# Kernel tuning notes

Hardware: AMD Instinct MI355X
Metric: run time of the kernel (lower is better)

The kernel has to match this reference:

```python
import jax, jax.numpy as jnp
import numpy as np

N, H, E, T, ED, AB = 50000, 64, 800000, 800000, 64, 16


def setup_inputs() -> dict:
    key = jax.random.key(0)
    ks = jax.random.split(key, 26)

    def nrm(k, shape, scale=1.0):
        return jax.random.normal(k, shape, dtype=jnp.float32) * scale

    d = {}
    d["s"] = nrm(ks[0], (N, H))
    d["v"] = nrm(ks[1], (N, H, 3))
    d["edge_index"] = jax.random.randint(ks[2], (2, E), 0, N, dtype=jnp.int32)
    d["edge_rbf"] = jax.random.uniform(ks[3], (E, ED), dtype=jnp.float32)
    raw_dir = jax.random.normal(ks[4], (E, 3), dtype=jnp.float32)
    d["edge_dir"] = raw_dir / jnp.linalg.norm(raw_dir, axis=-1, keepdims=True)
    d["triplet_kj"] = jax.random.randint(ks[5], (T,), 0, E, dtype=jnp.int32)
    d["triplet_ji"] = jax.random.randint(ks[6], (T,), 0, E, dtype=jnp.int32)
    d["angle_feat"] = jax.random.uniform(ks[7], (T, AB), dtype=jnp.float32)

    def lin(kw, kb, fan_in, fan_out):
        sc = 1.0 / np.sqrt(fan_in)
        return nrm(kw, (fan_in, fan_out), sc), nrm(kb, (fan_out,), sc)

    d["W_t1"], d["b_t1"] = lin(ks[8], ks[9], 2 * ED + AB, H)
    d["W_t2"], d["b_t2"] = lin(ks[10], ks[11], H, H)
    d["W_m1"], d["b_m1"] = lin(ks[12], ks[13], 2 * H + ED + H, H)
    d["W_m2"], d["b_m2"] = lin(ks[14], ks[15], H, 2 * H)
    d["W_u1"], d["b_u1"] = lin(ks[16], ks[17], 3 * H, H)
    d["W_u2"], d["b_u2"] = lin(ks[18], ks[19], H, H)
    d["W_g1"], d["b_g1"] = lin(ks[20], ks[21], 3 * H, H)
    d["W_g2"], d["b_g2"] = lin(ks[22], ks[23], H, H)
    d["ln_g"] = jnp.ones((H,), jnp.float32)
    d["ln_b"] = jnp.zeros((H,), jnp.float32)
    return d


def _mlp(x, W1, b1, W2, b2):
    return jax.nn.silu(x @ W1 + b1) @ W2 + b2


def reference(s, v, edge_index, edge_rbf, edge_dir, triplet_kj, triplet_ji,
              angle_feat, W_t1, b_t1, W_t2, b_t2, W_m1, b_m1, W_m2, b_m2,
              W_u1, b_u1, W_u2, b_u2, W_g1, b_g1, W_g2, b_g2, ln_g, ln_b):
    n_nodes, hid = s.shape
    n_edges = edge_rbf.shape[0]

    # 3-body triplet messages: gather two edge rbf rows + angle feature
    t_in = jnp.concatenate([edge_rbf[triplet_kj], edge_rbf[triplet_ji], angle_feat], axis=-1)
    t_msg = _mlp(t_in, W_t1, b_t1, W_t2, b_t2)                 # [T, H]
    angle_agg = jax.ops.segment_sum(t_msg, triplet_ji, num_segments=n_edges)  # [E, H]

    src, dst = edge_index[0], edge_index[1]
    msg_in = jnp.concatenate([s[src], s[dst], edge_rbf, angle_agg], axis=-1)  # [E, 4H]
    msg = _mlp(msg_in, W_m1, b_m1, W_m2, b_m2)                 # [E, 2H]
    m_s, m_v_coeff = jnp.split(msg, 2, axis=-1)

    agg_s = jax.ops.segment_sum(m_s, dst, num_segments=n_nodes)  # [N, H]
    m_v = m_v_coeff[:, :, None] * edge_dir[:, None, :]          # [E, H, 3]
    agg_v = jax.ops.segment_sum(m_v.reshape(n_edges, hid * 3), dst,
                                num_segments=n_nodes).reshape(n_nodes, hid, 3)

    v_norm = jnp.linalg.norm(v, axis=-1)                        # [N, H]
    ctx = jnp.concatenate([s, agg_s, v_norm], axis=-1)          # [N, 3H]
    s_new = s + _mlp(ctx, W_u1, b_u1, W_u2, b_u2)
    gate = jax.nn.sigmoid(_mlp(ctx, W_g1, b_g1, W_g2, b_g2))
    v_new = v + gate[..., None] * agg_v

    mu = s_new.mean(axis=-1, keepdims=True)
    var = s_new.var(axis=-1, keepdims=True)
    s_ln = (s_new - mu) / jnp.sqrt(var + 1e-5) * ln_g + ln_b
    s_out = jax.nn.silu(s_ln)
    return (s_out, v_new)
```

## Files before the change

kernel.cpp:

```cpp
#include <hip/hip_runtime.h>
#include <cstdint>
#include <cstddef>

#define NN 50000
#define NE 800000
#define NT 800000

typedef unsigned short u16;
typedef unsigned int u32;
typedef __attribute__((ext_vector_type(8))) short short8;
typedef __attribute__((ext_vector_type(4))) float f32x4;

__device__ __forceinline__ float silu_f(float x) { return x / (1.f + __expf(-x)); }
__device__ __forceinline__ float sigm_f(float x) { return 1.f / (1.f + __expf(-x)); }
__device__ __forceinline__ u16 f2b(float x) {
  u32 u = __float_as_uint(x);
  u32 r = u + 0x7fffu + ((u >> 16) & 1u);
  return (u16)(r >> 16);
}
__device__ __forceinline__ float b2f(u16 h) { return __uint_as_float(((u32)h) << 16); }
__device__ __forceinline__ u32 pk2(float a, float b) {
  return (u32)f2b(a) | ((u32)f2b(b) << 16);
}

template <int RW>
__device__ __forceinline__ int lx(int r, int c) {
  return r * RW + ((((c >> 3) ^ (r & 7)) << 3) | (c & 7));
}

__global__ __launch_bounds__(256) void kcvt_hist(
    const float* __restrict__ erbf, u16* __restrict__ erbf_bf,
    const float* __restrict__ s, u16* __restrict__ s_bf,
    const int* __restrict__ tji, const int* __restrict__ edst,
    int* __restrict__ tcnt, int* __restrict__ ncnt) {
  int i = blockIdx.x * 256 + threadIdx.x;
  const int NCVT = (NE + NN) * 16;
  if (i < NCVT) {
    const float* in; u16* out; int j;
    if (i < NE * 16) { in = erbf; out = erbf_bf; j = i; }
    else { in = s; out = s_bf; j = i - NE * 16; }
    float4 v = ((const float4*)in)[j];
    uint2 p;
    p.x = pk2(v.x, v.y);
    p.y = pk2(v.z, v.w);
    ((uint2*)out)[j] = p;
  } else {
    int j = i - NCVT;
    if (j < NT) atomicAdd(&tcnt[tji[j]], 1);
    else {
      j -= NT;
      if (j < NE) atomicAdd(&ncnt[edst[j]], 1);
    }
  }
}

__global__ __launch_bounds__(256) void kscan1b(
    const int* __restrict__ inA, int nA, int* __restrict__ outA, int* __restrict__ bsA, int BA,
    const int* __restrict__ inB, int nB, int* __restrict__ outB, int* __restrict__ bsB) {
  __shared__ int sh[256];
  const int* in; int n; int* out; int* bs; int blk;
  if ((int)blockIdx.x < BA) { in = inA; n = nA; out = outA; bs = bsA; blk = blockIdx.x; }
  else { in = inB; n = nB; out = outB; bs = bsB; blk = blockIdx.x - BA; }
  int tid = threadIdx.x;
  size_t base = (size_t)blk * 1024;
  int v[4];
  int acc = 0;
#pragma unroll
  for (int q = 0; q < 4; ++q) {
    size_t i = base + (size_t)tid * 4 + q;
    int x = (i < (size_t)n) ? in[i] : 0;
    v[q] = acc;
    acc += x;
  }
  sh[tid] = acc;
  __syncthreads();
  for (int off = 1; off < 256; off <<= 1) {
    int y = (tid >= off) ? sh[tid - off] : 0;
    __syncthreads();
    sh[tid] += y;
    __syncthreads();
  }
  int excl = (tid == 0) ? 0 : sh[tid - 1];
  if (tid == 255) bs[blk] = sh[255];
#pragma unroll
  for (int q = 0; q < 4; ++q) {
    size_t i = base + (size_t)tid * 4 + q;
    if (i < (size_t)n) out[i] = excl + v[q];
  }
}

__global__ __launch_bounds__(1024) void kscan2b(int* __restrict__ bsA, int nbA,
                                                int* __restrict__ bsB, int nbB) {
  __shared__ int sh[1024];
  int* bs = (blockIdx.x == 0) ? bsA : bsB;
  int nb = (blockIdx.x == 0) ? nbA : nbB;
  int tid = threadIdx.x;
  sh[tid] = (tid < nb) ? bs[tid] : 0;
  __syncthreads();
  for (int off = 1; off < 1024; off <<= 1) {
    int y = (tid >= off) ? sh[tid - off] : 0;
    __syncthreads();
    sh[tid] += y;
    __syncthreads();
  }
  if (tid < nb) bs[tid] = (tid == 0) ? 0 : sh[tid - 1];
}

__global__ __launch_bounds__(256) void kscan3b(
    int* __restrict__ outA, const int* __restrict__ bsA, int nA, int totalA,
    int* __restrict__ outB, const int* __restrict__ bsB, int nB, int totalB) {
  int i = blockIdx.x * 256 + threadIdx.x;
  if (i <= nA) {
    if (i < nA) outA[i] += bsA[i >> 10];
    else outA[nA] = totalA;
  } else {
    int j = i - (nA + 1);
    if (j < nB) outB[j] += bsB[j >> 10];
    else if (j == nB) outB[nB] = totalB;
  }
}

__global__ __launch_bounds__(256) void kprep_all(
    const int* __restrict__ tji, const int* __restrict__ toff, int* __restrict__ tcnt,
    int* __restrict__ tids, const float* __restrict__ afeat, u16* __restrict__ afeat_s,
    const int* __restrict__ edst, const int* __restrict__ noff, int* __restrict__ ncnt,
    int* __restrict__ eslot, const float* __restrict__ dir, float* __restrict__ dir_s,
    const float* __restrict__ Wt1, const float* __restrict__ Wt2,
    const float* __restrict__ Wm1, const float* __restrict__ Wm2,
    const float* __restrict__ Wu1, const float* __restrict__ Wu2,
    const float* __restrict__ Wg1, const float* __restrict__ Wg2,
    u16* __restrict__ Pt1, u16* __restrict__ Pt2,
    u16* __restrict__ Pm1, u16* __restrict__ Pm2,
    u16* __restrict__ Pu1, u16* __restrict__ Pu2,
    u16* __restrict__ Pg1, u16* __restrict__ Pg2) {
  int i = blockIdx.x * 256 + threadIdx.x;
  if (i < NT) {
    int k = tji[i];
    int slot = toff[k] + (atomicSub(&tcnt[k], 1) - 1);
    tids[slot] = i;
    const float4* src = (const float4*)(afeat + (size_t)i * 16);
    uint2* dst = (uint2*)(afeat_s + (size_t)slot * 16);
#pragma unroll
    for (int q = 0; q < 4; ++q) {
      float4 v = src[q];
      uint2 p;
      p.x = pk2(v.x, v.y);
      p.y = pk2(v.z, v.w);
      dst[q] = p;
    }
  } else if (i < NT + NE) {
    int j = i - NT;
    int k = edst[j];
    int slot = noff[k] + (atomicSub(&ncnt[k], 1) - 1);
    eslot[j] = slot;
    dir_s[(size_t)slot * 3 + 0] = dir[(size_t)j * 3 + 0];
    dir_s[(size_t)slot * 3 + 1] = dir[(size_t)j * 3 + 1];
    dir_s[(size_t)slot * 3 + 2] = dir[(size_t)j * 3 + 2];
  } else {
    int g = i - NT - NE;
    int f = g >> 6, l = g & 63;
    const float* W; u16* out; int K, N, fl;
    if (f < 20)       { W = Wt1; out = Pt1; K = 144; N = 64;  fl = f; }
    else if (f < 28)  { W = Wt2; out = Pt2; K = 64;  N = 64;  fl = f - 20; }
    else if (f < 60)  { W = Wm1; out = Pm1; K = 256; N = 64;  fl = f - 28; }
    else if (f < 76)  { W = Wm2; out = Pm2; K = 64;  N = 128; fl = f - 60; }
    else if (f < 100) { W = Wu1; out = Pu1; K = 192; N = 64;  fl = f - 76; }
    else if (f < 108) { W = Wu2; out = Pu2; K = 64;  N = 64;  fl = f - 100; }
    else if (f < 132) { W = Wg1; out = Pg1; K = 192; N = 64;  fl = f - 108; }
    else if (f < 140) { W = Wg2; out = Pg2; K = 64;  N = 64;  fl = f - 132; }
    else return;
    int nt = fl % (N / 16);
    int kt = fl / (N / 16);
    int k0 = kt * 32 + (l >> 4) * 8;
    int n = nt * 16 + (l & 15);
    u16 vals[8];
#pragma unroll
    for (int j = 0; j < 8; ++j) {
      int kk = k0 + j;
      vals[j] = (kk < K) ? f2b(W[(size_t)kk * N + n]) : (u16)0;
    }
    uint4* dst = (uint4*)(out + (size_t)fl * 512 + l * 8);
    uint4 p;
    p.x = (u32)vals[0] | ((u32)vals[1] << 16);
    p.y = (u32)vals[2] | ((u32)vals[3] << 16);
    p.z = (u32)vals[4] | ((u32)vals[5] << 16);
    p.w = (u32)vals[6] | ((u32)vals[7] << 16);
    *dst = p;
  }
}

__global__ __launch_bounds__(256) void ktrip_mfma(
    const int* __restrict__ tkj, const int* __restrict__ tji,
    const u16* __restrict__ erbf_bf, const u16* __restrict__ afeat_s,
    const int* __restrict__ tids,
    const u16* __restrict__ Wp1, const float* __restrict__ b1,
    const u16* __restrict__ Wp2, const float* __restrict__ b2,
    u16* __restrict__ tmsg_s) {
  __shared__ __align__(16) u16 Xs[64 * 192];
  u16* Hs = Xs + 64 * 128;
  const int tid = threadIdx.x;
  const int l = tid & 63;
  const int w = tid >> 6;
  const int st0 = blockIdx.x * 64;

#pragma unroll
  for (int it = 0; it < 4; ++it) {
    int idx = it * 256 + tid;
    int sel = idx >> 9, r = (idx >> 3) & 63, ch = idx & 7;
    int t = tids[st0 + r];
    int node = sel ? tji[t] : tkj[t];
    uint4 vv = *(const uint4*)&erbf_bf[(size_t)node * 64 + ch * 8];
    *(uint4*)&Xs[lx<192>(r, sel * 64 + ch * 8)] = vv;
  }
  {
    int r = tid >> 2, c = (tid & 3) * 4;
    uint2 p2 = *(const uint2*)&afeat_s[(size_t)(st0 + r) * 16 + c];
    *(uint2*)&Xs[lx<192>(r, 128 + c)] = p2;
  }
#pragma unroll
  for (int i = 0; i < 2; ++i) {
    int idx = i * 256 + tid;
    int r = idx >> 3, c = 144 + (idx & 7) * 2;
    *(u32*)&Xs[lx<192>(r, c)] = 0;
  }
  __syncthreads();

  f32x4 acc1[4];
  {
    float bias = b1[w * 16 + (l & 15)];
#pragma unroll
    for (int mt = 0; mt < 4; ++mt) acc1[mt] = (f32x4){bias, bias, bias, bias};
    for (int ks = 0; ks < 5; ++ks) {
      short8 bf = *(const short8*)(Wp1 + ((size_t)(ks * 4 + w) * 64 + l) * 8);
#pragma unroll
      for (int mt = 0; mt < 4; ++mt) {
        short8 af = *(const short8*)&Xs[lx<192>(mt * 16 + (l & 15), ks * 32 + ((l >> 4) << 3))];
        acc1[mt] = __builtin_amdgcn_mfma_f32_16x16x32_bf16(af, bf, acc1[mt], 0, 0, 0);
      }
    }
  }
  __syncthreads();
#pragma unroll
  for (int mt = 0; mt < 4; ++mt)
#pragma unroll
    for (int q = 0; q < 4; ++q) {
      int r = mt * 16 + (l >> 4) * 4 + q;
      Hs[lx<64>(r, w * 16 + (l & 15))] = f2b(silu_f(acc1[mt][q]));
    }
  __syncthreads();

  f32x4 acc2[4];
  {
    float bias = b2[w * 16 + (l & 15)];
#pragma unroll
    for (int mt = 0; mt < 4; ++mt) acc2[mt] = (f32x4){bias, bias, bias, bias};
    for (int ks = 0; ks < 2; ++ks) {
      short8 bf = *(const short8*)(Wp2 + ((size_t)(ks * 4 + w) * 64 + l) * 8);
#pragma unroll
      for (int mt = 0; mt < 4; ++mt) {
        short8 af = *(const short8*)&Hs[lx<64>(mt * 16 + (l & 15), ks * 32 + ((l >> 4) << 3))];
        acc2[mt] = __builtin_amdgcn_mfma_f32_16x16x32_bf16(af, bf, acc2[mt], 0, 0, 0);
      }
    }
  }
  __syncthreads();
#pragma unroll
  for (int mt = 0; mt < 4; ++mt)
#pragma unroll
    for (int q = 0; q < 4; ++q) {
      int r = mt * 16 + (l >> 4) * 4 + q;
      Xs[lx<64>(r, w * 16 + (l & 15))] = f2b(acc2[mt][q]);
    }
  __syncthreads();
  for (int i = 0; i < 2; ++i) {
    int idx = i * 256 + tid;
    int r = idx >> 3, c0 = (idx & 7) << 3;
    uint4 val = *(const uint4*)&Xs[lx<64>(r, c0)];
    *(uint4*)(tmsg_s + (size_t)(st0 + r) * 64 + c0) = val;
  }
}

__global__ __launch_bounds__(256) void kmsg_mfma(
    const int* __restrict__ eidx, const u16* __restrict__ s_bf,
    const u16* __restrict__ erbf_bf,
    const int* __restrict__ toff, const u16* __restrict__ tmsg_s,
    const int* __restrict__ eslot,
    const u16* __restrict__ Wp1, const float* __restrict__ b1,
    const u16* __restrict__ Wp2, const float* __restrict__ b2,
    u16* __restrict__ msg_s) {
  __shared__ __align__(16) u16 Xs[64 * 256];
  u16* Hs = Xs + 64 * 192;
  const int tid = threadIdx.x;
  const int l = tid & 63;
  const int w = tid >> 6;
  const int e0 = blockIdx.x * 64;

#pragma unroll
  for (int i = 0; i < 2; ++i) {
    int idx = i * 256 + tid;
    int r = idx >> 3, c0 = (idx & 7) << 3;
    uint4 vv = *(const uint4*)&erbf_bf[(size_t)(e0 + r) * 64 + c0];
    *(uint4*)&Xs[lx<256>(r, 128 + c0)] = vv;
  }
#pragma unroll
  for (int it = 0; it < 4; ++it) {
    int idx = it * 256 + tid;
    int sel = idx >> 9, r = (idx >> 3) & 63, ch = idx & 7;
    int node = eidx[sel * NE + e0 + r];
    uint4 vv = *(const uint4*)&s_bf[(size_t)node * 64 + ch * 8];
    *(uint4*)&Xs[lx<256>(r, sel * 64 + ch * 8)] = vv;
  }
#pragma unroll
  for (int it = 0; it < 2; ++it) {
    int idx = it * 256 + tid;
    int r = idx >> 3, ch = idx & 7;
    int e = e0 + r;
    int r0 = toff[e], r1 = toff[e + 1];
    float a[8];
#pragma unroll
    for (int j = 0; j < 8; ++j) a[j] = 0.f;
    for (int ri = r0; ri < r1; ++ri) {
      uint4 pk = *(const uint4*)&tmsg_s[(size_t)ri * 64 + ch * 8];
      a[0] += b2f((u16)(pk.x & 0xffff)); a[1] += b2f((u16)(pk.x >> 16));
      a[2] += b2f((u16)(pk.y & 0xffff)); a[3] += b2f((u16)(pk.y >> 16));
      a[4] += b2f((u16)(pk.z & 0xffff)); a[5] += b2f((u16)(pk.z >> 16));
      a[6] += b2f((u16)(pk.w & 0xffff)); a[7] += b2f((u16)(pk.w >> 16));
    }
    uint4 p;
    p.x = pk2(a[0], a[1]);
    p.y = pk2(a[2], a[3]);
    p.z = pk2(a[4], a[5]);
    p.w = pk2(a[6], a[7]);
    *(uint4*)&Xs[lx<256>(r, 192 + ch * 8)] = p;
  }
  __syncthreads();

  f32x4 acc1[4];
  {
    float bias = b1[w * 16 + (l & 15)];
#pragma unroll
    for (int mt = 0; mt < 4; ++mt) acc1[mt] = (f32x4){bias, bias, bias, bias};
    for (int ks = 0; ks < 8; ++ks) {
      short8 bf = *(const short8*)(Wp1 + ((size_t)(ks * 4 + w) * 64 + l) * 8);
#pragma unroll
      for (int mt = 0; mt < 4; ++mt) {
        short8 af = *(const short8*)&Xs[lx<256>(mt * 16 + (l & 15), ks * 32 + ((l >> 4) << 3))];
        acc1[mt] = __builtin_amdgcn_mfma_f32_16x16x32_bf16(af, bf, acc1[mt], 0, 0, 0);
      }
    }
  }
  __syncthreads();
#pragma unroll
  for (int mt = 0; mt < 4; ++mt)
#pragma unroll
    for (int q = 0; q < 4; ++q) {
      int r = mt * 16 + (l >> 4) * 4 + q;
      Hs[lx<64>(r, w * 16 + (l & 15))] = f2b(silu_f(acc1[mt][q]));
    }
  __syncthreads();

  f32x4 acc2[2][4];
#pragma unroll
  for (int pp = 0; pp < 2; ++pp) {
    int nt = w * 2 + pp;
    float bias = b2[nt * 16 + (l & 15)];
#pragma unroll
    for (int mt = 0; mt < 4; ++mt) acc2[pp][mt] = (f32x4){bias, bias, bias, bias};
    for (int ks = 0; ks < 2; ++ks) {
      short8 bf = *(const short8*)(Wp2 + ((size_t)(ks * 8 + nt) * 64 + l) * 8);
#pragma unroll
      for (int mt = 0; mt < 4; ++mt) {
        short8 af = *(const short8*)&Hs[lx<64>(mt * 16 + (l & 15), ks * 32 + ((l >> 4) << 3))];
        acc2[pp][mt] = __builtin_amdgcn_mfma_f32_16x16x32_bf16(af, bf, acc2[pp][mt], 0, 0, 0);
      }
    }
  }
  __syncthreads();
#pragma unroll
  for (int pp = 0; pp < 2; ++pp)
#pragma unroll
    for (int mt = 0; mt < 4; ++mt)
#pragma unroll
      for (int q = 0; q < 4; ++q) {
        int r = mt * 16 + (l >> 4) * 4 + q;
        Xs[lx<128>(r, (w * 2 + pp) * 16 + (l & 15))] = f2b(acc2[pp][mt][q]);
      }
  __syncthreads();
  for (int i = 0; i < 4; ++i) {
    int idx = i * 256 + tid;
    int r = idx >> 4, c0 = (idx & 15) << 3;
    int slot = eslot[e0 + r];
    uint4 val = *(const uint4*)&Xs[lx<128>(r, c0)];
    *(uint4*)(msg_s + (size_t)slot * 128 + c0) = val;
  }
}

__global__ __launch_bounds__(256) void kagg(
    const int* __restrict__ noff, const u16* __restrict__ msg_s,
    const float* __restrict__ dir_s,
    u16* __restrict__ aggs_bf, float* __restrict__ aggv) {
  const int lane = threadIdx.x & 63;
  const int wv = threadIdx.x >> 6;
  const int n = blockIdx.x * 4 + wv;
  if (n >= NN) return;
  const int r0 = noff[n], r1 = noff[n + 1];
  const int lrow = lane >> 4, lcol = lane & 15;
  const bool is_ms = (lcol < 8);

  float a[8];
  float v0[8], v1[8], v2[8];
#pragma unroll
  for (int j = 0; j < 8; ++j) { a[j] = 0.f; v0[j] = 0.f; v1[j] = 0.f; v2[j] = 0.f; }

  for (int r4 = r0; r4 < r1; r4 += 4) {
    int r = r4 + lrow;
    if (r < r1) {
      uint4 pk = *(const uint4*)&msg_s[(size_t)r * 128 + lcol * 8];
      float x[8];
      x[0] = b2f((u16)(pk.x & 0xffff)); x[1] = b2f((u16)(pk.x >> 16));
      x[2] = b2f((u16)(pk.y & 0xffff)); x[3] = b2f((u16)(pk.y >> 16));
      x[4] = b2f((u16)(pk.z & 0xffff)); x[5] = b2f((u16)(pk.z >> 16));
      x[6] = b2f((u16)(pk.w & 0xffff)); x[7] = b2f((u16)(pk.w >> 16));
      if (is_ms) {
#pragma unroll
        for (int j = 0; j < 8; ++j) a[j] += x[j];
      } else {
        float dx = dir_s[(size_t)r * 3 + 0];
        float dy = dir_s[(size_t)r * 3 + 1];
        float dz = dir_s[(size_t)r * 3 + 2];
#pragma unroll
        for (int j = 0; j < 8; ++j) {
          v0[j] += x[j] * dx; v1[j] += x[j] * dy; v2[j] += x[j] * dz;
        }
      }
    }
  }
#pragma unroll
  for (int j = 0; j < 8; ++j) {
    a[j] += __shfl_xor(a[j], 16);  a[j] += __shfl_xor(a[j], 32);
    v0[j] += __shfl_xor(v0[j], 16); v0[j] += __shfl_xor(v0[j], 32);
    v1[j] += __shfl_xor(v1[j], 16); v1[j] += __shfl_xor(v1[j], 32);
    v2[j] += __shfl_xor(v2[j], 16); v2[j] += __shfl_xor(v2[j], 32);
  }
  if (lrow == 0) {
    if (is_ms) {
      uint4 p;
      p.x = pk2(a[0], a[1]);
      p.y = pk2(a[2], a[3]);
      p.z = pk2(a[4], a[5]);
      p.w = pk2(a[6], a[7]);
      *(uint4*)&aggs_bf[(size_t)n * 64 + lcol * 8] = p;
    } else {
      int c0 = (lcol - 8) * 8;
      float* av = aggv + (size_t)n * 192 + (size_t)c0 * 3;
      float4 o0 = {v0[0], v1[0], v2[0], v0[1]};
      float4 o1 = {v1[1], v2[1], v0[2], v1[2]};
      float4 o2 = {v2[2], v0[3], v1[3], v2[3]};
      float4 o3 = {v0[4], v1[4], v2[4], v0[5]};
      float4 o4 = {v1[5], v2[5], v0[6], v1[6]};
      float4 o5 = {v2[6], v0[7], v1[7], v2[7]};
      float4* av4 = (float4*)av;
      av4[0] = o0; av4[1] = o1; av4[2] = o2; av4[3] = o3; av4[4] = o4; av4[5] = o5;
    }
  }
}

__global__ __launch_bounds__(256) void knode_mfma(
    const u16* __restrict__ s_bf, const float* __restrict__ v,
    const u16* __restrict__ aggs_bf, const float* __restrict__ aggv,
    const u16* __restrict__ WpU1, const float* __restrict__ bU1,
    const u16* __restrict__ WpU2, const float* __restrict__ bU2,
    const u16* __restrict__ WpG1, const float* __restrict__ bG1,
    const u16* __restrict__ WpG2, const float* __restrict__ bG2,
    const float* __restrict__ lng, const float* __restrict__ lnb,
    float* __restrict__ outs, float* __restrict__ outv) {
  __shared__ __align__(16) char smem[64 * 192 * 2 + 2 * 64 * 64 * 2];
  u16* Xs = (u16*)smem;
  u16* Hu = (u16*)(smem + 64 * 192 * 2);
  u16* Hg = Hu + 64 * 64;
  float* Fs = (float*)smem;

  const int tid = threadIdx.x;
  const int l = tid & 63;
  const int w = tid >> 6;
  const int n0 = blockIdx.x * 64;

  for (int i = 0; i < 2; ++i) {
    int idx = i * 256 + tid;
    int r = idx >> 3, c0 = (idx & 7) << 3;
    int nr = n0 + r; if (nr >= NN) nr = NN - 1;
    uint4 a = *(const uint4*)&s_bf[(size_t)nr * 64 + c0];
    *(uint4*)&Xs[lx<192>(r, c0)] = a;
    uint4 b = *(const uint4*)&aggs_bf[(size_t)nr * 64 + c0];
    *(uint4*)&Xs[lx<192>(r, 64 + c0)] = b;
  }
  for (int it = 0; it < 16; ++it) {
    int idx = it * 256 + tid;
    int r = idx >> 6, c = idx & 63;
    int nr = n0 + r; if (nr >= NN) nr = NN - 1;
    const float* vp = v + (size_t)nr * 192 + c * 3;
    float x = vp[0], y = vp[1], z = vp[2];
    Xs[lx<192>(r, 128 + c)] = f2b(sqrtf(x * x + y * y + z * z));
  }
  __syncthreads();

  f32x4 au[4], ag[4];
  {
    float biu = bU1[w * 16 + (l & 15)], big = bG1[w * 16 + (l & 15)];
#pragma unroll
    for (int mt = 0; mt < 4; ++mt) {
      au[mt] = (f32x4){biu, biu, biu, biu};
      ag[mt] = (f32x4){big, big, big, big};
    }
    for (int ks = 0; ks < 6; ++ks) {
      short8 bu = *(const short8*)(WpU1 + ((size_t)(ks * 4 + w) * 64 + l) * 8);
      short8 bg = *(const short8*)(WpG1 + ((size_t)(ks * 4 + w) * 64 + l) * 8);
#pragma unroll
      for (int mt = 0; mt < 4; ++mt) {
        short8 af = *(const short8*)&Xs[lx<192>(mt * 16 + (l & 15), ks * 32 + ((l >> 4) << 3))];
        au[mt] = __builtin_amdgcn_mfma_f32_16x16x32_bf16(af, bu, au[mt], 0, 0, 0);
        ag[mt] = __builtin_amdgcn_mfma_f32_16x16x32_bf16(af, bg, ag[mt], 0, 0, 0);
      }
    }
  }
#pragma unroll
  for (int mt = 0; mt < 4; ++mt)
#pragma unroll
    for (int q = 0; q < 4; ++q) {
      int r = mt * 16 + (l >> 4) * 4 + q;
      Hu[lx<64>(r, w * 16 + (l & 15))] = f2b(silu_f(au[mt][q]));
      Hg[lx<64>(r, w * 16 + (l & 15))] = f2b(silu_f(ag[mt][q]));
    }
  __syncthreads();

  f32x4 ou[4], og[4];
  {
    float biu = bU2[w * 16 + (l & 15)], big = bG2[w * 16 + (l & 15)];
#pragma unroll
    for (int mt = 0; mt < 4; ++mt) {
      ou[mt] = (f32x4){biu, biu, biu, biu};
      og[mt] = (f32x4){big, big, big, big};
    }
    for (int ks = 0; ks < 2; ++ks) {
      short8 bu = *(const short8*)(WpU2 + ((size_t)(ks * 4 + w) * 64 + l) * 8);
      short8 bg = *(const short8*)(WpG2 + ((size_t)(ks * 4 + w) * 64 + l) * 8);
#pragma unroll
      for (int mt = 0; mt < 4; ++mt) {
        short8 afu = *(const short8*)&Hu[lx<64>(mt * 16 + (l & 15), ks * 32 + ((l >> 4) << 3))];
        ou[mt] = __builtin_amdgcn_mfma_f32_16x16x32_bf16(afu, bu, ou[mt], 0, 0, 0);
        short8 afg = *(const short8*)&Hg[lx<64>(mt * 16 + (l & 15), ks * 32 + ((l >> 4) << 3))];
        og[mt] = __builtin_amdgcn_mfma_f32_16x16x32_bf16(afg, bg, og[mt], 0, 0, 0);
      }
    }
  }
#pragma unroll
  for (int mt = 0; mt < 4; ++mt)
#pragma unroll
    for (int q = 0; q < 4; ++q) {
      int r = mt * 16 + (l >> 4) * 4 + q;
      ou[mt][q] += b2f(Xs[lx<192>(r, w * 16 + (l & 15))]);
    }
  __syncthreads();

#pragma unroll
  for (int mt = 0; mt < 4; ++mt)
#pragma unroll
    for (int q = 0; q < 4; ++q) {
      int r = mt * 16 + (l >> 4) * 4 + q;
      Fs[r * 68 + w * 16 + (l & 15)] = ou[mt][q];
    }
  __syncthreads();
  {
    int r = tid >> 2, c0 = (tid & 3) * 16;
    float xv[16];
#pragma unroll
    for (int j4 = 0; j4 < 4; ++j4) {
      float4 t = *(const float4*)&Fs[r * 68 + c0 + j4 * 4];
      xv[j4 * 4 + 0] = t.x; xv[j4 * 4 + 1] = t.y;
      xv[j4 * 4 + 2] = t.z; xv[j4 * 4 + 3] = t.w;
    }
    float sm = 0.f, sq = 0.f;
#pragma unroll
    for (int j = 0; j < 16; ++j) { sm += xv[j]; sq += xv[j] * xv[j]; }
    sm += __shfl_xor(sm, 1); sq += __shfl_xor(sq, 1);
    sm += __shfl_xor(sm, 2); sq += __shfl_xor(sq, 2);
    float mu = sm * (1.f / 64.f);
    float var = sq * (1.f / 64.f) - mu * mu;
    float rstd = rsqrtf(var + 1e-5f);
    if (n0 + r < NN) {
      float* op = outs + (size_t)(n0 + r) * 64 + c0;
#pragma unroll
      for (int j4 = 0; j4 < 4; ++j4) {
        float4 o;
        float y0 = (xv[j4 * 4 + 0] - mu) * rstd * lng[c0 + j4 * 4 + 0] + lnb[c0 + j4 * 4 + 0];
        float y1 = (xv[j4 * 4 + 1] - mu) * rstd * lng[c0 + j4 * 4 + 1] + lnb[c0 + j4 * 4 + 1];
        float y2 = (xv[j4 * 4 + 2] - mu) * rstd * lng[c0 + j4 * 4 + 2] + lnb[c0 + j4 * 4 + 2];
        float y3 = (xv[j4 * 4 + 3] - mu) * rstd * lng[c0 + j4 * 4 + 3] + lnb[c0 + j4 * 4 + 3];
        o.x = silu_f(y0); o.y = silu_f(y1); o.z = silu_f(y2); o.w = silu_f(y3);
        *(float4*)(op + j4 * 4) = o;
      }
    }
  }
  __syncthreads();

#pragma unroll
  for (int mt = 0; mt < 4; ++mt)
#pragma unroll
    for (int q = 0; q < 4; ++q) {
      int r = mt * 16 + (l >> 4) * 4 + q;
      Fs[r * 68 + w * 16 + (l & 15)] = og[mt][q];
    }
  __syncthreads();
  {
    int r = tid >> 2, c0 = (tid & 3) * 16;
    int nr = n0 + r;
    if (nr < NN) {
      float gate[16];
#pragma unroll
      for (int j = 0; j < 16; ++j) gate[j] = sigm_f(Fs[r * 68 + c0 + j]);
      const float4* vp = (const float4*)(v + (size_t)nr * 192 + c0 * 3);
      const float4* ap = (const float4*)(aggv + (size_t)nr * 192 + c0 * 3);
      float4* op = (float4*)(outv + (size_t)nr * 192 + c0 * 3);
#pragma unroll
      for (int j4 = 0; j4 < 12; ++j4) {
        float4 vv = vp[j4], av = ap[j4], o;
        o.x = vv.x + gate[(j4 * 4 + 0) / 3] * av.x;
        o.y = vv.y + gate[(j4 * 4 + 1) / 3] * av.y;
        o.z = vv.z + gate[(j4 * 4 + 2) / 3] * av.z;
        o.w = vv.w + gate[(j4 * 4 + 3) / 3] * av.w;
        op[j4] = o;
      }
    }
  }
}

extern "C" void kernel_launch(void* const* d_in, const int* in_sizes, int n_in,
                              void* d_out, int out_size, void* d_ws, size_t ws_size,
                              hipStream_t stream) {
  const float* s     = (const float*)d_in[0];
  const float* v     = (const float*)d_in[1];
  const int*   eidx  = (const int*)d_in[2];
  const float* erbf  = (const float*)d_in[3];
  const float* edir  = (const float*)d_in[4];
  const int*   tkj   = (const int*)d_in[5];
  const int*   tji   = (const int*)d_in[6];
  const float* afeat = (const float*)d_in[7];
  const float* W_t1  = (const float*)d_in[8];
  const float* b_t1  = (const float*)d_in[9];
  const float* W_t2  = (const float*)d_in[10];
  const float* b_t2  = (const float*)d_in[11];
  const float* W_m1  = (const float*)d_in[12];
  const float* b_m1  = (const float*)d_in[13];
  const float* W_m2  = (const float*)d_in[14];
  const float* b_m2  = (const float*)d_in[15];
  const float* W_u1  = (const float*)d_in[16];
  const float* b_u1  = (const float*)d_in[17];
  const float* W_u2  = (const float*)d_in[18];
  const float* b_u2  = (const float*)d_in[19];
  const float* W_g1  = (const float*)d_in[20];
  const float* b_g1  = (const float*)d_in[21];
  const float* W_g2  = (const float*)d_in[22];
  const float* b_g2  = (const float*)d_in[23];
  const float* ln_g  = (const float*)d_in[24];
  const float* ln_b  = (const float*)d_in[25];

  char* w = (char*)d_ws;
  auto alloc = [&](size_t bytes) -> char* {
    char* p = w;
    w += (bytes + 255) & ~(size_t)255;
    return p;
  };
  int* tcnt  = (int*)alloc((size_t)NE * 4);
  int* ncnt  = (int*)alloc((size_t)NN * 4);
  size_t zspan = (size_t)((char*)(ncnt + NN) - (char*)tcnt);
  int* toff  = (int*)alloc((size_t)(NE + 1) * 4);
  int* noff  = (int*)alloc((size_t)(NN + 1) * 4);
  int* tids  = (int*)alloc((size_t)NT * 4);
  int* eslot = (int*)alloc((size_t)NE * 4);
  int* bsum  = (int*)alloc(2048 * 4);
  float* dir_s = (float*)alloc((size_t)NE * 3 * 4);
  u16* msg_s  = (u16*)alloc((size_t)NE * 128 * 2);
  u16* tmsg_s = (u16*)alloc((size_t)NT * 64 * 2);
  u16* erbf_bf = (u16*)alloc((size_t)NE * 64 * 2);
  u16* s_bf    = (u16*)alloc((size_t)NN * 64 * 2);
  u16* Wp_t1 = (u16*)alloc((size_t)5 * 4 * 512 * 2);
  u16* Wp_t2 = (u16*)alloc((size_t)2 * 4 * 512 * 2);
  u16* Wp_m1 = (u16*)alloc((size_t)8 * 4 * 512 * 2);
  u16* Wp_m2 = (u16*)alloc((size_t)2 * 8 * 512 * 2);
  u16* Wp_u1 = (u16*)alloc((size_t)6 * 4 * 512 * 2);
  u16* Wp_u2 = (u16*)alloc((size_t)2 * 4 * 512 * 2);
  u16* Wp_g1 = (u16*)alloc((size_t)6 * 4 * 512 * 2);
  u16* Wp_g2 = (u16*)alloc((size_t)2 * 4 * 512 * 2);
  u16* afeat_s = msg_s;
  float* aggv = (float*)tmsg_s;
  u16* aggs_bf = tmsg_s + (size_t)NN * 384;

  hipMemsetAsync(tcnt, 0, zspan, stream);

  kcvt_hist<<<((NE + NN) * 16 + NT + NE + 255) / 256, 256, 0, stream>>>(
      erbf, erbf_bf, s, s_bf, tji, eidx + NE, tcnt, ncnt);

  const int Bt = (NE + 1023) / 1024, Bn = (NN + 1023) / 1024;
  kscan1b<<<Bt + Bn, 256, 0, stream>>>(tcnt, NE, toff, bsum, Bt, ncnt, NN, noff, bsum + 1024);
  kscan2b<<<2, 1024, 0, stream>>>(bsum, Bt, bsum + 1024, Bn);
  kscan3b<<<(NE + 1 + NN + 1 + 255) / 256, 256, 0, stream>>>(toff, bsum, NE, NT,
                                                             noff, bsum + 1024, NN, NE);

  kprep_all<<<(NT + NE + 140 * 64 + 255) / 256, 256, 0, stream>>>(
      tji, toff, tcnt, tids, afeat, afeat_s,
      eidx + NE, noff, ncnt, eslot, edir, dir_s,
      W_t1, W_t2, W_m1, W_m2, W_u1, W_u2, W_g1, W_g2,
      Wp_t1, Wp_t2, Wp_m1, Wp_m2, Wp_u1, Wp_u2, Wp_g1, Wp_g2);

  ktrip_mfma<<<NT / 64, 256, 0, stream>>>(tkj, tji, erbf_bf, afeat_s, tids,
                                          Wp_t1, b_t1, Wp_t2, b_t2, tmsg_s);
  kmsg_mfma<<<NE / 64, 256, 0, stream>>>(eidx, s_bf, erbf_bf, toff, tmsg_s, eslot,
                                         Wp_m1, b_m1, Wp_m2, b_m2, msg_s);
  kagg<<<(NN + 3) / 4, 256, 0, stream>>>(noff, msg_s, dir_s, aggs_bf, aggv);

  float* out_s = (float*)d_out;
  float* out_v = out_s + (size_t)NN * 64;
  knode_mfma<<<(NN + 63) / 64, 256, 0, stream>>>(s_bf, v, aggs_bf, aggv,
                                                 Wp_u1, b_u1, Wp_u2, b_u2,
                                                 Wp_g1, b_g1, Wp_g2, b_g2,
                                                 ln_g, ln_b, out_s, out_v);
}
```

Measured before the change: 620.0 us.

## Gather edge and node rows straight into LDS with global_load_lds

The triplet and message MLP kernels now gather bf16 rows with the direct global-to-LDS load builtin instead of loading into registers and then storing to shared memory. The shared buffer is split into separate 64-column swizzled panels, and the source chunk index is pre-swizzled so the existing XOR layout is preserved. The first-layer K loops are fully unrolled to pick the panel per step. This is meant to cut VGPR staging and LDS write instructions on the gather path. It relies on the compiler waiting for the async LDS loads to complete before the barrier, and on the 16-byte variant being available on gfx950.

Result: no change. 608.6 us (-1.8%).

```diff
diff --git a/kernel.cpp b/kernel.cpp
--- a/kernel.cpp
+++ b/kernel.cpp
@@ -26,6 +26,11 @@
 template <int RW>
 __device__ __forceinline__ int lx(int r, int c) {
   return r * RW + ((((c >> 3) ^ (r & 7)) << 3) | (c & 7));
+}
+
+__device__ __forceinline__ void gload16(const void* g, void* l) {
+  __builtin_amdgcn_global_load_lds((const __attribute__((address_space(1))) void*)g,
+                                   (__attribute__((address_space(3))) void*)l, 16, 0, 0);
 }
 
 __global__ __launch_bounds__(256) void kcvt_hist(
@@ -196,32 +201,36 @@
     const u16* __restrict__ Wp1, const float* __restrict__ b1,
     const u16* __restrict__ Wp2, const float* __restrict__ b2,
     u16* __restrict__ tmsg_s) {
-  __shared__ __align__(16) u16 Xs[64 * 192];
-  u16* Hs = Xs + 64 * 128;
+  __shared__ __align__(16) u16 S[3][64 * 64];
+  u16* Hs = &S[0][0];
+  u16* OS = &S[1][0];
   const int tid = threadIdx.x;
   const int l = tid & 63;
   const int w = tid >> 6;
   const int st0 = blockIdx.x * 64;
 
-#pragma unroll
-  for (int it = 0; it < 4; ++it) {
-    int idx = it * 256 + tid;
-    int sel = idx >> 9, r = (idx >> 3) & 63, ch = idx & 7;
-    int t = tids[st0 + r];
-    int node = sel ? tji[t] : tkj[t];
-    uint4 vv = *(const uint4*)&erbf_bf[(size_t)node * 64 + ch * 8];
-    *(uint4*)&Xs[lx<192>(r, sel * 64 + ch * 8)] = vv;
+  {
+    int wr = w * 16;
+#pragma unroll
+    for (int v = 0; v < 2; ++v) {
+      int br = wr + v * 8;
+      int r = br + (l >> 3);
+      int sch = (l & 7) ^ (r & 7);
+      int t = tids[st0 + r];
+      gload16(erbf_bf + (size_t)tkj[t] * 64 + sch * 8, &S[0][br * 64]);
+      gload16(erbf_bf + (size_t)tji[t] * 64 + sch * 8, &S[1][br * 64]);
+    }
   }
   {
     int r = tid >> 2, c = (tid & 3) * 4;
     uint2 p2 = *(const uint2*)&afeat_s[(size_t)(st0 + r) * 16 + c];
-    *(uint2*)&Xs[lx<192>(r, 128 + c)] = p2;
+    *(uint2*)&S[2][lx<64>(r, c)] = p2;
   }
 #pragma unroll
   for (int i = 0; i < 2; ++i) {
     int idx = i * 256 + tid;
-    int r = idx >> 3, c = 144 + (idx & 7) * 2;
-    *(u32*)&Xs[lx<192>(r, c)] = 0;
+    int r = idx >> 3, c = 16 + (idx & 7) * 2;
+    *(u32*)&S[2][lx<64>(r, c)] = 0;
   }
   __syncthreads();
 
@@ -230,11 +239,14 @@
     float bias = b1[w * 16 + (l & 15)];
 #pragma unroll
     for (int mt = 0; mt < 4; ++mt) acc1[mt] = (f32x4){bias, bias, bias, bias};
+#pragma unroll
     for (int ks = 0; ks < 5; ++ks) {
       short8 bf = *(const short8*)(Wp1 + ((size_t)(ks * 4 + w) * 64 + l) * 8);
+      const u16* R = &S[ks >> 1][0];
+      int cc = (ks & 1) * 32 + ((l >> 4) << 3);
 #pragma unroll
       for (int mt = 0; mt < 4; ++mt) {
-        short8 af = *(const short8*)&Xs[lx<192>(mt * 16 + (l & 15), ks * 32 + ((l >> 4) << 3))];
+        short8 af = *(const short8*)&R[lx<64>(mt * 16 + (l & 15), cc)];
         acc1[mt] = __builtin_amdgcn_mfma_f32_16x16x32_bf16(af, bf, acc1[mt], 0, 0, 0);
       }
     }
@@ -269,13 +281,13 @@
 #pragma unroll
     for (int q = 0; q < 4; ++q) {
       int r = mt * 16 + (l >> 4) * 4 + q;
-      Xs[lx<64>(r, w * 16 + (l & 15))] = f2b(acc2[mt][q]);
+      OS[lx<64>(r, w * 16 + (l & 15))] = f2b(acc2[mt][q]);
     }
   __syncthreads();
   for (int i = 0; i < 2; ++i) {
     int idx = i * 256 + tid;
     int r = idx >> 3, c0 = (idx & 7) << 3;
-    uint4 val = *(const uint4*)&Xs[lx<64>(r, c0)];
+    uint4 val = *(const uint4*)&OS[lx<64>(r, c0)];
     *(uint4*)(tmsg_s + (size_t)(st0 + r) * 64 + c0) = val;
   }
 }
@@ -288,27 +300,25 @@
     const u16* __restrict__ Wp1, const float* __restrict__ b1,
     const u16* __restrict__ Wp2, const float* __restrict__ b2,
     u16* __restrict__ msg_s) {
-  __shared__ __align__(16) u16 Xs[64 * 256];
-  u16* Hs = Xs + 64 * 192;
+  __shared__ __align__(16) u16 S[4][64 * 64];
+  u16* Hs = &S[0][0];
+  u16* OS = &S[1][0];
   const int tid = threadIdx.x;
   const int l = tid & 63;
   const int w = tid >> 6;
   const int e0 = blockIdx.x * 64;
 
-#pragma unroll
-  for (int i = 0; i < 2; ++i) {
-    int idx = i * 256 + tid;
-    int r = idx >> 3, c0 = (idx & 7) << 3;
-    uint4 vv = *(const uint4*)&erbf_bf[(size_t)(e0 + r) * 64 + c0];
-    *(uint4*)&Xs[lx<256>(r, 128 + c0)] = vv;
-  }
-#pragma unroll
-  for (int it = 0; it < 4; ++it) {
-    int idx = it * 256 + tid;
-    int sel = idx >> 9, r = (idx >> 3) & 63, ch = idx & 7;
-    int node = eidx[sel * NE + e0 + r];
-    uint4 vv = *(const uint4*)&s_bf[(size_t)node * 64 + ch * 8];
-    *(uint4*)&Xs[lx<256>(r, sel * 64 + ch * 8)] = vv;
+  {
+    int wr = w * 16;
+#pragma unroll
+    for (int v = 0; v < 2; ++v) {
+      int br = wr + v * 8;
+      int r = br + (l >> 3);
+      int sch = (l & 7) ^ (r & 7);
+      gload16(s_bf + (size_t)eidx[e0 + r] * 64 + sch * 8, &S[0][br * 64]);
+      gload16(s_bf + (size_t)eidx[NE + e0 + r] * 64 + sch * 8, &S[1][br * 64]);
+      gload16(erbf_bf + (size_t)(e0 + r) * 64 + sch * 8, &S[2][br * 64]);
+    }
   }
 #pragma unroll
   for (int it = 0; it < 2; ++it) {
@@ -331,7 +341,7 @@
     p.y = pk2(a[2], a[3]);
     p.z = pk2(a[4], a[5]);
     p.w = pk2(a[6], a[7]);
-    *(uint4*)&Xs[lx<256>(r, 192 + ch * 8)] = p;
+    *(uint4*)&S[3][lx<64>(r, ch * 8)] = p;
   }
   __syncthreads();
 
@@ -340,11 +350,14 @@
     float bias = b1[w * 16 + (l & 15)];
 #pragma unroll
     for (int mt = 0; mt < 4; ++mt) acc1[mt] = (f32x4){bias, bias, bias, bias};
+#pragma unroll
     for (int ks = 0; ks < 8; ++ks) {
       short8 bf = *(const short8*)(Wp1 + ((size_t)(ks * 4 + w) * 64 + l) * 8);
+      const u16* R = &S[ks >> 1][0];
+      int cc = (ks & 1) * 32 + ((l >> 4) << 3);
 #pragma unroll
       for (int mt = 0; mt < 4; ++mt) {
-        short8 af = *(const short8*)&Xs[lx<256>(mt * 16 + (l & 15), ks * 32 + ((l >> 4) << 3))];
+        short8 af = *(const short8*)&R[lx<64>(mt * 16 + (l & 15), cc)];
         acc1[mt] = __builtin_amdgcn_mfma_f32_16x16x32_bf16(af, bf, acc1[mt], 0, 0, 0);
       }
     }
@@ -383,14 +396,14 @@
 #pragma unroll
       for (int q = 0; q < 4; ++q) {
         int r = mt * 16 + (l >> 4) * 4 + q;
-        Xs[lx<128>(r, (w * 2 + pp) * 16 + (l & 15))] = f2b(acc2[pp][mt][q]);
+        OS[lx<128>(r, (w * 2 + pp) * 16 + (l & 15))] = f2b(acc2[pp][mt][q]);
       }
   __syncthreads();
   for (int i = 0; i < 4; ++i) {
     int idx = i * 256 + tid;
     int r = idx >> 4, c0 = (idx & 15) << 3;
     int slot = eslot[e0 + r];
-    uint4 val = *(const uint4*)&Xs[lx<128>(r, c0)];
+    uint4 val = *(const uint4*)&OS[lx<128>(r, c0)];
     *(uint4*)(msg_s + (size_t)slot * 128 + c0) = val;
   }
 }
```
